# Kernel tuning notes

Hardware: AMD Instinct MI355X
Metric: run time of the kernel (lower is better)

## Reference

```python
import jax, jax.numpy as jnp
import numpy as np

D = 2048
NUM_HEADS = 16
HEAD_DIM = D // NUM_HEADS
B, T = 4, 2048
NEG = -1e9


def setup_inputs() -> dict:
    key = jax.random.key(0)
    ks = jax.random.split(key, 6)
    X = jax.random.normal(ks[0], (B, T, D), dtype=jnp.float32)
    # additive causal mask, broadcast over batch and heads
    causal = jnp.tril(jnp.ones((T, T), dtype=jnp.float32))
    mask = jnp.where(causal == 1, 0.0, NEG)[None, None, :, :]
    scale = np.sqrt(2.0 / D).astype(np.float32)
    wq_w = jax.random.normal(ks[1], (D, D), dtype=jnp.float32) * scale
    wk_w = jax.random.normal(ks[2], (D, D), dtype=jnp.float32) * scale
    wv_w = jax.random.normal(ks[3], (D, D), dtype=jnp.float32) * scale
    wo_w = jax.random.normal(ks[4], (D, D), dtype=jnp.float32) * scale
    zeros = jnp.zeros((D,), dtype=jnp.float32)
    return {
        "X": X, "mask": mask,
        "wq_w": wq_w, "wq_b": zeros,
        "wk_w": wk_w, "wk_b": zeros,
        "wv_w": wv_w, "wv_b": zeros,
        "wo_w": wo_w, "wo_b": zeros,
    }


def reference(X, mask, wq_w, wq_b, wk_w, wk_b, wv_w, wv_b, wo_w, wo_b):
    b, t, d = X.shape
    # project and split heads: [b, h, t, hd]
    def proj(w, bias):
        return (X @ w + bias).reshape(b, t, NUM_HEADS, HEAD_DIM).transpose(0, 2, 1, 3)
    Q = proj(wq_w, wq_b)
    K = proj(wk_w, wk_b)
    V = proj(wv_w, wv_b)
    scores = jnp.einsum("bhqd,bhkd->bhqk", Q, K) / np.sqrt(HEAD_DIM).astype(X.dtype)
    scores = scores + mask
    A = jax.nn.softmax(scores, axis=-1)
    ctx = jnp.einsum("bhqk,bhkd->bhqd", A, V)  # [b, h, t, hd]
    ctx = ctx.transpose(0, 2, 1, 3).reshape(b, t, d)
    return ctx @ wo_w + wo_b
```

## Files before the change

### kernel.cpp

```cpp
#include <hip/hip_runtime.h>
#include <stdint.h>

#define DMODEL 2048
#define NH 16
#define HD 128
#define BATCH 4
#define SEQ 2048
#define MTOT (BATCH * SEQ)
#define LOG2E 1.44269504088896340736f

typedef __bf16 bf16x8 __attribute__((ext_vector_type(8)));
typedef float floatx4 __attribute__((ext_vector_type(4)));

__device__ __forceinline__ uint16_t f2b(float f) {
    union { float f; uint32_t i; } v; v.f = f;
    uint32_t r = v.i + 0x7fffu + ((v.i >> 16) & 1u);
    return (uint16_t)(r >> 16);
}

#define GLD16(gp, lp)                                                          \
    __builtin_amdgcn_global_load_lds(                                          \
        (__attribute__((address_space(1))) unsigned int*)(gp),                 \
        (__attribute__((address_space(3))) unsigned int*)(lp), 16, 0, 0)

__global__ __launch_bounds__(256) void cvt_bf16(const float* __restrict__ in,
                                                uint16_t* __restrict__ out, int n) {
    const int i = (blockIdx.x * 256 + threadIdx.x) * 8;
    if (i >= n) return;
    const float4 a = *(const float4*)(in + i);
    const float4 b = *(const float4*)(in + i + 4);
    uint16_t v[8] __attribute__((aligned(16))) = {
        f2b(a.x), f2b(a.y), f2b(a.z), f2b(a.w),
        f2b(b.x), f2b(b.y), f2b(b.z), f2b(b.w)};
    *(uint4*)(out + i) = *(const uint4*)v;
}

__global__ __launch_bounds__(256) void tr_wf(const float* __restrict__ in,
                                             uint16_t* __restrict__ out) {
    __shared__ float t[64 * 69];
    const int tid = threadIdx.x;
    const int r0 = blockIdx.y * 64, c0 = blockIdx.x * 64;
    const int rr = tid >> 2, c16 = (tid & 3) << 4;
#pragma unroll
    for (int j = 0; j < 4; j++)
        *(float4*)&t[rr * 69 + c16 + j * 4] =
            *(const float4*)(in + (size_t)(r0 + rr) * DMODEL + c0 + c16 + j * 4);
    __syncthreads();
    const int oc = tid >> 2, r16 = (tid & 3) << 4;
    uint16_t v[16] __attribute__((aligned(16)));
#pragma unroll
    for (int j = 0; j < 16; j++) v[j] = f2b(t[(r16 + j) * 69 + oc]);
    uint16_t* o = out + (size_t)(c0 + oc) * DMODEL + r0 + r16;
    *(uint4*)o = *(const uint4*)v;
    *(uint4*)(o + 8) = *(const uint4*)(v + 8);
}

__global__ __launch_bounds__(256, 2) void gemm(const uint16_t* __restrict__ A,
                                               const uint16_t* __restrict__ Bt,
                                               const float* __restrict__ bias,
                                               void* __restrict__ Cout,
                                               float scale, int mode, int tld) {
    __shared__ __attribute__((aligned(16))) uint16_t As[128 * 32];
    __shared__ __attribute__((aligned(16))) uint16_t Bs[128 * 32];
    const int tid = threadIdx.x, lane = tid & 63, w = tid >> 6;
    const int wr = w >> 1, wc = w & 1;
    const int col = lane & 15, quad = lane >> 4;
    const long m0 = (long)blockIdx.y * 128, n0 = (long)blockIdx.x * 128;

    floatx4 acc[4][4];
#pragma unroll
    for (int i = 0; i < 4; i++)
#pragma unroll
        for (int j = 0; j < 4; j++) acc[i][j] = (floatx4){0.f, 0.f, 0.f, 0.f};

    const int srow = tid >> 2, sc = (tid & 3) << 3;
    const uint16_t* Ag0 = A + (m0 + srow) * DMODEL + sc;
    const uint16_t* Bg0 = Bt + (n0 + srow) * DMODEL + sc;
    const long rstep = (long)64 * DMODEL;
    uint16_t* AsW = &As[w * 512];
    uint16_t* BsW = &Bs[w * 512];

    for (int kt = 0; kt < DMODEL; kt += 32) {
        GLD16(Ag0 + kt, AsW);
        GLD16(Ag0 + rstep + kt, AsW + 2048);
        GLD16(Bg0 + kt, BsW);
        GLD16(Bg0 + rstep + kt, BsW + 2048);
        __syncthreads();
        bf16x8 af[4], bfr[4];
#pragma unroll
        for (int i = 0; i < 4; i++)
            af[i] = *(const bf16x8*)&As[(wr * 64 + i * 16 + col) * 32 + quad * 8];
#pragma unroll
        for (int j = 0; j < 4; j++)
            bfr[j] = *(const bf16x8*)&Bs[(wc * 64 + j * 16 + col) * 32 + quad * 8];
#pragma unroll
        for (int i = 0; i < 4; i++)
#pragma unroll
            for (int j = 0; j < 4; j++)
                acc[i][j] = __builtin_amdgcn_mfma_f32_16x16x32_bf16(af[i], bfr[j],
                                                                    acc[i][j], 0, 0, 0);
        __syncthreads();
    }

    float bv[4];
#pragma unroll
    for (int j = 0; j < 4; j++) bv[j] = bias[n0 + wc * 64 + j * 16 + col];
#pragma unroll
    for (int i = 0; i < 4; i++) {
        const long row = m0 + wr * 64 + i * 16 + quad * 4;
#pragma unroll
        for (int j = 0; j < 4; j++) {
            const long cc = n0 + wc * 64 + j * 16 + col;
            if (mode == 2) {
                uint16_t tmp[4] __attribute__((aligned(8)));
#pragma unroll
                for (int r = 0; r < 4; r++)
                    tmp[r] = f2b((acc[i][j][r] + bv[j]) * scale);
                *(uint2*)&((uint16_t*)Cout)[(size_t)cc * tld + row] =
                    *(const uint2*)tmp;
            } else {
#pragma unroll
                for (int r = 0; r < 4; r++) {
                    const float v = (acc[i][j][r] + bv[j]) * scale;
                    const long idx = (row + r) * DMODEL + cc;
                    if (mode == 1) ((float*)Cout)[idx] = v;
                    else           ((uint16_t*)Cout)[idx] = f2b(v);
                }
            }
        }
    }
}

__global__ __launch_bounds__(256, 2) void flash(uint16_t* __restrict__ QO,
                                                const uint16_t* __restrict__ Kp,
                                                const uint16_t* __restrict__ Vt,
                                                int vld) {
    __shared__ __attribute__((aligned(16))) uint16_t Ks[16 * 512];
    __shared__ __attribute__((aligned(16))) uint16_t Vs[16 * 512];
    __shared__ __attribute__((aligned(16))) uint16_t Ps[4][32 * 88];

    const int tid = threadIdx.x, lane = tid & 63, w = tid >> 6;
    const int col = lane & 15, quad = lane >> 4;
    const int h = blockIdx.y & 15, b = blockIdx.y >> 4;
    const size_t brow = (size_t)b * SEQ;

    const uint16_t* kbase = Kp + brow * DMODEL + h * HD;
    const uint16_t* vtbase = Vt + (size_t)(h * HD) * vld + brow;
    const uint16_t* kg0 = kbase + (size_t)(w * 16 + col) * DMODEL + quad * 8;
    const uint16_t* vg0 = vtbase + (size_t)(w * 32 + col) * vld + quad * 8;

    for (int half = 0; half < 2; ++half) {
        const int qi = half ? (int)blockIdx.x : (15 - (int)blockIdx.x);
        const int q0 = qi * 128;
        uint16_t* qbase = QO + (brow + q0 + w * 32) * DMODEL + h * HD;

        bf16x8 qf[2][4];
#pragma unroll
        for (int i = 0; i < 2; i++)
#pragma unroll
            for (int kk = 0; kk < 4; kk++)
                qf[i][kk] = *(const bf16x8*)(qbase + (size_t)(i * 16 + col) * DMODEL +
                                             kk * 32 + quad * 8);

        floatx4 accO[2][8];
#pragma unroll
        for (int i = 0; i < 2; i++)
#pragma unroll
            for (int jd = 0; jd < 8; jd++) accO[i][jd] = (floatx4){0.f, 0.f, 0.f, 0.f};
        float mrun[2][4], lrun[2][4];
#pragma unroll
        for (int i = 0; i < 2; i++)
#pragma unroll
            for (int r = 0; r < 4; r++) { mrun[i][r] = -1e30f; lrun[i][r] = 0.f; }

        const int nkt = 2 * qi + 2;

        uint4 kv[4], vv4[4];
        {
#pragma unroll
            for (int p = 0; p < 4; p++)
                kv[p] = *(const uint4*)(kg0 + p * 32);
#pragma unroll
            for (int s = 0; s < 2; s++)
#pragma unroll
                for (int k2 = 0; k2 < 2; k2++)
                    vv4[s * 2 + k2] =
                        *(const uint4*)(vg0 + (size_t)s * 16 * vld + k2 * 32);
        }

        for (int ki = 0; ki < nkt; ki++) {
            const int key0 = ki * 64;
#pragma unroll
            for (int p = 0; p < 4; p++)
                *(uint4*)&Ks[(w * 4 + p) * 512 + lane * 8] = kv[p];
#pragma unroll
            for (int s = 0; s < 2; s++)
#pragma unroll
                for (int k2 = 0; k2 < 2; k2++)
                    *(uint4*)&Vs[((w * 2 + s) * 2 + k2) * 512 + lane * 8] =
                        vv4[s * 2 + k2];
            __syncthreads();

            if (ki + 1 < nkt) {
                const size_t koff = (size_t)(key0 + 64);
#pragma unroll
                for (int p = 0; p < 4; p++)
                    kv[p] = *(const uint4*)(kg0 + koff * DMODEL + p * 32);
#pragma unroll
                for (int s = 0; s < 2; s++)
#pragma unroll
                    for (int k2 = 0; k2 < 2; k2++)
                        vv4[s * 2 + k2] = *(const uint4*)(vg0 + (size_t)s * 16 * vld +
                                                          koff + k2 * 32);
            }

            floatx4 s[2][4];
            __builtin_amdgcn_s_setprio(1);
#pragma unroll
            for (int i = 0; i < 2; i++)
#pragma unroll
                for (int jk = 0; jk < 4; jk++) {
                    floatx4 a = (floatx4){0.f, 0.f, 0.f, 0.f};
#pragma unroll
                    for (int kk = 0; kk < 4; kk++) {
                        bf16x8 bb = *(const bf16x8*)&Ks[(jk * 4 + kk) * 512 + lane * 8];
                        a = __builtin_amdgcn_mfma_f32_16x16x32_bf16(qf[i][kk], bb, a, 0, 0, 0);
                    }
                    s[i][jk] = a;
                }
            __builtin_amdgcn_s_setprio(0);

            if (key0 + 63 > q0 + w * 32) {
#pragma unroll
                for (int i = 0; i < 2; i++) {
                    const int qb = q0 + w * 32 + i * 16 + quad * 4;
#pragma unroll
                    for (int jk = 0; jk < 4; jk++) {
                        const int key = key0 + jk * 16 + col;
#pragma unroll
                        for (int r = 0; r < 4; r++)
                            if (key > qb + r) s[i][jk][r] = -1e30f;
                    }
                }
            }

            float alpha[2][4];
#pragma unroll
            for (int i = 0; i < 2; i++)
#pragma unroll
                for (int r = 0; r < 4; r++) {
                    float mx = s[i][0][r];
#pragma unroll
                    for (int jk = 1; jk < 4; jk++) mx = fmaxf(mx, s[i][jk][r]);
                    mx = fmaxf(mx, __shfl_xor(mx, 1, 64));
                    mx = fmaxf(mx, __shfl_xor(mx, 2, 64));
                    mx = fmaxf(mx, __shfl_xor(mx, 4, 64));
                    mx = fmaxf(mx, __shfl_xor(mx, 8, 64));
                    mx = fmaxf(mx, mrun[i][r]);
                    alpha[i][r] = exp2f((mrun[i][r] - mx) * LOG2E);
                    mrun[i][r] = mx;
                }
#pragma unroll
            for (int i = 0; i < 2; i++)
#pragma unroll
                for (int r = 0; r < 4; r++) {
                    float psum = 0.f;
#pragma unroll
                    for (int jk = 0; jk < 4; jk++) {
                        const float p = exp2f((s[i][jk][r] - mrun[i][r]) * LOG2E);
                        psum += p;
                        Ps[w][(i * 16 + quad * 4 + r) * 88 + jk * 16 + col] = f2b(p);
                    }
                    lrun[i][r] = lrun[i][r] * alpha[i][r] + psum;
                }
#pragma unroll
            for (int i = 0; i < 2; i++)
#pragma unroll
                for (int jd = 0; jd < 8; jd++)
#pragma unroll
                    for (int r = 0; r < 4; r++) accO[i][jd][r] *= alpha[i][r];

            bf16x8 pf[2][2];
#pragma unroll
            for (int i = 0; i < 2; i++)
#pragma unroll
                for (int k2 = 0; k2 < 2; k2++)
                    pf[i][k2] = *(const bf16x8*)&Ps[w][(i * 16 + col) * 88 + k2 * 32 + quad * 8];
            __builtin_amdgcn_s_setprio(1);
#pragma unroll
            for (int jd = 0; jd < 8; jd++)
#pragma unroll
                for (int k2 = 0; k2 < 2; k2++) {
                    bf16x8 vvv = *(const bf16x8*)&Vs[(jd * 2 + k2) * 512 + lane * 8];
#pragma unroll
                    for (int i = 0; i < 2; i++)
                        accO[i][jd] = __builtin_amdgcn_mfma_f32_16x16x32_bf16(pf[i][k2], vvv,
                                                                              accO[i][jd], 0, 0, 0);
                }
            __builtin_amdgcn_s_setprio(0);
            __syncthreads();
        }

        float inv[2][4];
#pragma unroll
        for (int i = 0; i < 2; i++)
#pragma unroll
            for (int r = 0; r < 4; r++) {
                float l = lrun[i][r];
                l += __shfl_xor(l, 1, 64);
                l += __shfl_xor(l, 2, 64);
                l += __shfl_xor(l, 4, 64);
                l += __shfl_xor(l, 8, 64);
                inv[i][r] = 1.0f / l;
            }
#pragma unroll
        for (int i = 0; i < 2; i++)
#pragma unroll
            for (int jd = 0; jd < 8; jd++)
#pragma unroll
                for (int r = 0; r < 4; r++)
                    qbase[(size_t)(i * 16 + quad * 4 + r) * DMODEL + jd * 16 + col] =
                        f2b(accO[i][jd][r] * inv[i][r]);
    }
}

extern "C" void kernel_launch(void* const* d_in, const int* in_sizes, int n_in,
                              void* d_out, int out_size, void* d_ws, size_t ws_size,
                              hipStream_t stream) {
    const float* X   = (const float*)d_in[0];
    float*       msk = (float*)d_in[1];
    const float* wq  = (const float*)d_in[2];
    const float* wqb = (const float*)d_in[3];
    const float* wk  = (const float*)d_in[4];
    const float* wkb = (const float*)d_in[5];
    const float* wv  = (const float*)d_in[6];
    const float* wvb = (const float*)d_in[7];
    const float* wo  = (const float*)d_in[8];
    const float* wob = (const float*)d_in[9];
    float* out = (float*)d_out;

    char* ws = (char*)d_ws;
    const size_t MB = 1ull << 20;
    dim3 tb(256), gT(32, 32);
    const float qs = 0.08838834764831845f;

    if (ws_size >= 136 * MB) {
        uint16_t* Xb = (uint16_t*)(ws);
        uint16_t* Qb = (uint16_t*)(ws + 32 * MB);
        uint16_t* Kb = (uint16_t*)(ws + 64 * MB);
        uint16_t* Vb = (uint16_t*)(ws + 96 * MB);
        uint16_t* Wt = (uint16_t*)(ws + 128 * MB);
        dim3 gG(16, 64), gF(8, 64);
        cvt_bf16<<<8192, tb, 0, stream>>>(X, Xb, MTOT * DMODEL);
        tr_wf<<<gT, tb, 0, stream>>>(wq, Wt);
        gemm<<<gG, tb, 0, stream>>>(Xb, Wt, wqb, Qb, qs, 0, 0);
        tr_wf<<<gT, tb, 0, stream>>>(wk, Wt);
        gemm<<<gG, tb, 0, stream>>>(Xb, Wt, wkb, Kb, 1.0f, 0, 0);
        tr_wf<<<gT, tb, 0, stream>>>(wv, Wt);
        gemm<<<gG, tb, 0, stream>>>(Xb, Wt, wvb, Vb, 1.0f, 2, MTOT);
        flash<<<gF, tb, 0, stream>>>(Qb, Kb, Vb, MTOT);
        tr_wf<<<gT, tb, 0, stream>>>(wo, Wt);
        gemm<<<gG, tb, 0, stream>>>(Qb, Wt, wob, out, 1.0f, 1, 0);
    } else {
        uint16_t* Xb = (uint16_t*)(ws);
        uint16_t* Qb = (uint16_t*)(ws + 8 * MB);
        uint16_t *Kb, *Vb, *Wt;
        if (ws_size >= 40 * MB) {
            Kb = (uint16_t*)(ws + 16 * MB);
            Vb = (uint16_t*)(ws + 24 * MB);
            Wt = (uint16_t*)(ws + 32 * MB);
        } else {
            Kb = (uint16_t*)msk;
            Vb = Kb + (size_t)SEQ * DMODEL;
            Wt = (uint16_t*)(ws + 16 * MB);
        }
        dim3 gG(16, 16), gF(8, 16);
        for (int b = 0; b < BATCH; b++) {
            const float* Xf = X + (size_t)b * SEQ * DMODEL;
            float* Ob = out + (size_t)b * SEQ * DMODEL;
            cvt_bf16<<<2048, tb, 0, stream>>>(Xf, Xb, SEQ * DMODEL);
            tr_wf<<<gT, tb, 0, stream>>>(wq, Wt);
            gemm<<<gG, tb, 0, stream>>>(Xb, Wt, wqb, Qb, qs, 0, 0);
            tr_wf<<<gT, tb, 0, stream>>>(wk, Wt);
            gemm<<<gG, tb, 0, stream>>>(Xb, Wt, wkb, Kb, 1.0f, 0, 0);
            tr_wf<<<gT, tb, 0, stream>>>(wv, Wt);
            gemm<<<gG, tb, 0, stream>>>(Xb, Wt, wvb, Vb, 1.0f, 2, SEQ);
            flash<<<gF, tb, 0, stream>>>(Qb, Kb, Vb, SEQ);
            tr_wf<<<gT, tb, 0, stream>>>(wo, Wt);
            gemm<<<gG, tb, 0, stream>>>(Qb, Wt, wob, Ob, 1.0f, 1, 0);
        }
    }

    (void)in_sizes; (void)n_in; (void)out_size;
}
```

Baseline: 735.2 us.

## Add 256x256-tile double-buffered GEMM with 512 threads for projections

Introduces a new GEMM kernel using 256x256 output tiles, 8 waves, a 64-wide K step with double-buffered LDS filled by direct global-to-LDS loads, and an XCD-aware block swizzle. It replaces the 128x128 GEMM for all four projections on the large-workspace path. The aim is more reuse per loaded byte and overlap of loads with MFMA work. The cost is higher register and LDS use (128 KB LDS per block), which limits occupancy, and the 256 tile gives fewer blocks per launch.

```diff
diff --git a/kernel.cpp b/kernel.cpp
--- a/kernel.cpp
+++ b/kernel.cpp
@@ -22,6 +22,13 @@
     __builtin_amdgcn_global_load_lds(                                          \
         (__attribute__((address_space(1))) unsigned int*)(gp),                 \
         (__attribute__((address_space(3))) unsigned int*)(lp), 16, 0, 0)
+
+#define WAITVMC(N) asm volatile("s_waitcnt vmcnt(" #N ")" ::: "memory")
+#define WAITLGKM0                                                              \
+    do {                                                                       \
+        asm volatile("s_waitcnt lgkmcnt(0)" ::: "memory");                     \
+        __builtin_amdgcn_sched_barrier(0);                                     \
+    } while (0)
 
 __global__ __launch_bounds__(256) void cvt_bf16(const float* __restrict__ in,
                                                 uint16_t* __restrict__ out, int n) {
@@ -53,6 +60,120 @@
     uint16_t* o = out + (size_t)(c0 + oc) * DMODEL + r0 + r16;
     *(uint4*)o = *(const uint4*)v;
     *(uint4*)(o + 8) = *(const uint4*)(v + 8);
+}
+
+__global__ __launch_bounds__(512, 2) void gemm256(const uint16_t* __restrict__ A,
+                                                  const uint16_t* __restrict__ Bt,
+                                                  const float* __restrict__ bias,
+                                                  void* __restrict__ Cout,
+                                                  float scale, int mode, int tld) {
+    __shared__ __attribute__((aligned(16))) uint16_t As[2][32 * 512];
+    __shared__ __attribute__((aligned(16))) uint16_t Bs[2][32 * 512];
+
+    const int tid = threadIdx.x, lane = tid & 63, w = tid >> 6;
+    const int wr = w >> 2, wc = w & 3;
+    const int col = lane & 15, quad = lane >> 4;
+
+    const int nwg = gridDim.x, cpx = nwg >> 3;
+    const int swz = ((int)blockIdx.x & 7) * cpx + ((int)blockIdx.x >> 3);
+    const long m0 = (long)(swz >> 3) * 256;
+    const long n0 = (long)(swz & 7) * 256;
+
+    const uint16_t* Ab = A + (m0 + col) * (size_t)DMODEL + quad * 8;
+    const uint16_t* Bb = Bt + (n0 + col) * (size_t)DMODEL + quad * 8;
+
+#define STAGE256(bf, kt)                                                       \
+    {                                                                          \
+        const size_t kb = (size_t)(kt) * 64;                                   \
+        _Pragma("unroll") for (int j = 0; j < 4; j++) {                        \
+            const int blk = w * 4 + j;                                         \
+            const size_t off =                                                 \
+                kb + (size_t)(blk >> 1) * (16 * DMODEL) + (size_t)(blk & 1) * 32; \
+            GLD16(Ab + off, &As[bf][blk * 512]);                               \
+            GLD16(Bb + off, &Bs[bf][blk * 512]);                               \
+        }                                                                      \
+    }
+
+    floatx4 acc[8][4];
+#pragma unroll
+    for (int m = 0; m < 8; m++)
+#pragma unroll
+        for (int n = 0; n < 4; n++) acc[m][n] = (floatx4){0.f, 0.f, 0.f, 0.f};
+
+    const int NT = DMODEL / 64;
+    STAGE256(0, 0);
+    STAGE256(1, 1);
+
+#pragma unroll 1
+    for (int kt = 0; kt < NT; ++kt) {
+        const int cur = kt & 1;
+        if (kt == NT - 1) { WAITVMC(0); } else { WAITVMC(8); }
+        __builtin_amdgcn_s_barrier();
+
+        bf16x8 a0[8], b0[4];
+#pragma unroll
+        for (int m = 0; m < 8; m++)
+            a0[m] = *(const bf16x8*)&As[cur][((wr * 8 + m) * 2 + 0) * 512 + lane * 8];
+#pragma unroll
+        for (int n = 0; n < 4; n++)
+            b0[n] = *(const bf16x8*)&Bs[cur][((wc * 4 + n) * 2 + 0) * 512 + lane * 8];
+        __builtin_amdgcn_s_setprio(1);
+#pragma unroll
+        for (int m = 0; m < 8; m++)
+#pragma unroll
+            for (int n = 0; n < 4; n++)
+                acc[m][n] = __builtin_amdgcn_mfma_f32_16x16x32_bf16(a0[m], b0[n],
+                                                                    acc[m][n], 0, 0, 0);
+        __builtin_amdgcn_s_setprio(0);
+
+        bf16x8 a1[8], b1[4];
+#pragma unroll
+        for (int m = 0; m < 8; m++)
+            a1[m] = *(const bf16x8*)&As[cur][((wr * 8 + m) * 2 + 1) * 512 + lane * 8];
+#pragma unroll
+        for (int n = 0; n < 4; n++)
+            b1[n] = *(const bf16x8*)&Bs[cur][((wc * 4 + n) * 2 + 1) * 512 + lane * 8];
+        WAITLGKM0;
+        __builtin_amdgcn_s_barrier();
+        if (kt + 2 < NT) STAGE256(cur, kt + 2);
+        __builtin_amdgcn_s_setprio(1);
+#pragma unroll
+        for (int m = 0; m < 8; m++)
+#pragma unroll
+            for (int n = 0; n < 4; n++)
+                acc[m][n] = __builtin_amdgcn_mfma_f32_16x16x32_bf16(a1[m], b1[n],
+                                                                    acc[m][n], 0, 0, 0);
+        __builtin_amdgcn_s_setprio(0);
+    }
+
+    float bv[4];
+#pragma unroll
+    for (int n = 0; n < 4; n++) bv[n] = bias[n0 + wc * 64 + n * 16 + col];
+#pragma unroll
+    for (int m = 0; m < 8; m++) {
+        const long row = m0 + wr * 128 + m * 16 + quad * 4;
+#pragma unroll
+        for (int n = 0; n < 4; n++) {
+            const long cc = n0 + wc * 64 + n * 16 + col;
+            if (mode == 2) {
+                uint16_t tmp[4] __attribute__((aligned(8)));
+#pragma unroll
+                for (int r = 0; r < 4; r++)
+                    tmp[r] = f2b((acc[m][n][r] + bv[n]) * scale);
+                *(uint2*)&((uint16_t*)Cout)[(size_t)cc * tld + row] =
+                    *(const uint2*)tmp;
+            } else {
+#pragma unroll
+                for (int r = 0; r < 4; r++) {
+                    const float v = (acc[m][n][r] + bv[n]) * scale;
+                    const long idx = (row + r) * DMODEL + cc;
+                    if (mode == 1) ((float*)Cout)[idx] = v;
+                    else           ((uint16_t*)Cout)[idx] = f2b(v);
+                }
+            }
+        }
+    }
+#undef STAGE256
 }
 
 __global__ __launch_bounds__(256, 2) void gemm(const uint16_t* __restrict__ A,
@@ -341,7 +462,7 @@
 
     char* ws = (char*)d_ws;
     const size_t MB = 1ull << 20;
-    dim3 tb(256), gT(32, 32);
+    dim3 tb(256), tb512(512), gT(32, 32);
     const float qs = 0.08838834764831845f;
 
     if (ws_size >= 136 * MB) {
@@ -350,17 +471,18 @@
         uint16_t* Kb = (uint16_t*)(ws + 64 * MB);
         uint16_t* Vb = (uint16_t*)(ws + 96 * MB);
         uint16_t* Wt = (uint16_t*)(ws + 128 * MB);
-        dim3 gG(16, 64), gF(8, 64);
+        dim3 g256((MTOT / 256) * (DMODEL / 256));
+        dim3 gF(8, 64);
         cvt_bf16<<<8192, tb, 0, stream>>>(X, Xb, MTOT * DMODEL);
         tr_wf<<<gT, tb, 0, stream>>>(wq, Wt);
-        gemm<<<gG, tb, 0, stream>>>(Xb, Wt, wqb, Qb, qs, 0, 0);
+        gemm256<<<g256, tb512, 0, stream>>>(Xb, Wt, wqb, Qb, qs, 0, 0);
         tr_wf<<<gT, tb, 0, stream>>>(wk, Wt);
-        gemm<<<gG, tb, 0, stream>>>(Xb, Wt, wkb, Kb, 1.0f, 0, 0);
+        gemm256<<<g256, tb512, 0, stream>>>(Xb, Wt, wkb, Kb, 1.0f, 0, 0);
         tr_wf<<<gT, tb, 0, stream>>>(wv, Wt);
-        gemm<<<gG, tb, 0, stream>>>(Xb, Wt, wvb, Vb, 1.0f, 2, MTOT);
+        gemm256<<<g256, tb512, 0, stream>>>(Xb, Wt, wvb, Vb, 1.0f, 2, MTOT);
         flash<<<gF, tb, 0, stream>>>(Qb, Kb, Vb, MTOT);
         tr_wf<<<gT, tb, 0, stream>>>(wo, Wt);
-        gemm<<<gG, tb, 0, stream>>>(Qb, Wt, wob, out, 1.0f, 1, 0);
+        gemm256<<<g256, tb512, 0, stream>>>(Qb, Wt, wob, out, 1.0f, 1, 0);
     } else {
         uint16_t* Xb = (uint16_t*)(ws);
         uint16_t* Qb = (uint16_t*)(ws + 8 * MB);
```

New measurement: 752.6 us. 1.02x slower.
